# Kernel tuning notes

Measured on AMD Instinct MI355X. Metric: run time of the kernel, lower is better.

## Reference

```python
import jax, jax.numpy as jnp
import numpy as np

B, M, TP2, H, K, S = 64, 1, 1024, 256, 128, 1024
EPS = 2.220446049250313e-16  # numpy.finfo(float).eps


def setup_inputs() -> dict:
    key = jax.random.key(0)
    ks = jax.random.split(key, 12)
    inp = {
        'event': jax.random.randint(ks[0], (B, M, TP2), 0, K + 3),
        'dtime': jax.random.uniform(ks[1], (B, M, TP2), jnp.float32),
        'post': jax.random.uniform(ks[2], (B, M), jnp.float32),
        'duration': jax.random.uniform(ks[3], (B, M), jnp.float32),
        'dtime_sampling': jax.random.uniform(ks[4], (B, M, S), jnp.float32),
        'index_of_hidden_sampling': jax.random.randint(ks[5], (B, M, S), 0, B * M * (TP2 - 1)),
        'mask_sampling': jnp.ones((B, M, S), jnp.float32),
        # learned parameters
        'Emb': jax.random.normal(ks[6], (K + 3, H), jnp.float32) * 0.05,
        'W': jax.random.normal(ks[7], (7 * H, 2 * H), jnp.float32) * (1.0 / np.sqrt(2 * H)),
        'b': jnp.zeros((7 * H,), jnp.float32),
        'Wl': jax.random.normal(ks[8], (K, H), jnp.float32) * (1.0 / np.sqrt(H)),
    }
    return inp


def reference(event, dtime, post, duration, dtime_sampling, index_of_hidden_sampling,
              mask_sampling, Emb, W, b, Wl):
    Bs, Ms, Tp2 = event.shape
    Hd = Emb.shape[1]
    Tp1 = Tp2 - 1
    emb = Emb[event[:, :, :-1]]            # (B,M,T+1,H)
    dts = dtime[:, :, 1:]                  # (B,M,T+1)
    xs = (jnp.moveaxis(emb, 2, 0), jnp.moveaxis(dts, 2, 0))

    def step(carry, x):
        h, c, cbar = carry
        e, dt = x
        z = jnp.concatenate([e, h], axis=-1) @ W.T + b  # (B,M,7H)
        gi, gf, go, gz, gib, gfb, gd = jnp.split(z, 7, axis=-1)
        gi, gf, go = jax.nn.sigmoid(gi), jax.nn.sigmoid(gf), jax.nn.sigmoid(go)
        gib, gfb = jax.nn.sigmoid(gib), jax.nn.sigmoid(gfb)
        zc = jnp.tanh(gz)
        gd = jax.nn.softplus(gd)  # beta = 1
        c_i = gf * c + gi * zc
        cbar_i = gfb * cbar + gib * zc
        h_plus = go * jnp.tanh(c_i)  # decay with dtime = 0
        c_next = cbar_i + (c_i - cbar_i) * jnp.exp(-gd * dt[..., None])
        h_next = go * jnp.tanh(c_next)
        return (h_next, c_next, cbar_i), (c_i, cbar_i, gd, go, h_next)

    init = tuple(jnp.zeros((Bs, Ms, Hd), dtime.dtype) for _ in range(3))
    _, outs = jax.lax.scan(step, init, xs)
    all_c, all_cb, all_gd, all_go, all_h = (jnp.moveaxis(a, 0, 2) for a in outs)  # (B,M,T+1,H)

    # target + mask (getTarget)
    Kn = Wl.shape[0]
    tgt_raw = event[:, :, 1:]
    mask_complete = (tgt_raw < Kn).astype(dtime.dtype)
    tgt = jnp.where(tgt_raw < Kn, tgt_raw, 0)

    # log-intensity at events (getLogLambda)
    lam = jax.nn.softplus(all_h @ Wl.T)                        # (B,M,T+1,K)
    log_lam = jnp.log(lam + EPS)
    log_lam_tgt = jnp.take_along_axis(log_lam, tgt[..., None], axis=3)[..., 0] * mask_complete

    # sampled states (getSampledStates)
    idx = index_of_hidden_sampling.reshape(-1)
    Sn = dtime_sampling.shape[2]
    gather = lambda a: a.reshape(Bs * Ms * Tp1, Hd)[idx].reshape(Bs, Ms, Sn, Hd)
    cs, cbs, gds, gos = gather(all_c), gather(all_cb), gather(all_gd), gather(all_go)
    c_samp = cbs + (cs - cbs) * jnp.exp(-gds * dtime_sampling[..., None])
    hy = gos * jnp.tanh(c_samp)

    # MC integral (getIntegral)
    lam_s = jax.nn.softplus(hy @ Wl.T).sum(3)                  # (B,M,S)
    lam_mean = (lam_s * mask_sampling).sum(2) / mask_sampling.sum(2)
    integral = lam_mean * duration

    # complete log-likelihood per (batch, particle)
    loglik = log_lam_tgt.sum(2) - integral                     # (B,M)
    return loglik
```

## Files before the change

kernel.cpp:

```cpp
#include <hip/hip_runtime.h>
#include <hip/hip_fp16.h>
#include <cstdint>
#include <cstddef>

#define EPSF 2.220446049250313e-16f

#define Bn   64
#define TP2n 1024
#define Tn   1023
#define Hn   256
#define H7n  1792
#define Kn   128
#define NEn  131

typedef _Float16 f16x2 __attribute__((ext_vector_type(2)));
typedef unsigned uintx4 __attribute__((ext_vector_type(4)));

__device__ __forceinline__ f16x2 u2h(unsigned u) { return __builtin_bit_cast(f16x2, u); }
__device__ __forceinline__ f16x2 f2h(float f)    { return __builtin_bit_cast(f16x2, f); }

__device__ __forceinline__ int sdot4f(unsigned a, unsigned b, int c) {
#if __has_builtin(__builtin_amdgcn_sdot4)
  return __builtin_amdgcn_sdot4((int)a, (int)b, c, false);
#else
  int r = c;
#pragma unroll
  for (int i = 0; i < 4; ++i) {
    int av = ((int)(a << (24 - 8 * i))) >> 24;
    int bv = ((int)(b << (24 - 8 * i))) >> 24;
    r += av * bv;
  }
  return r;
#endif
}

__device__ __forceinline__ float sigmf(float x) { return 1.f / (1.f + __expf(-x)); }

__device__ __forceinline__ float tanhfast(float x) {
  float t = __expf(2.f * fabsf(x));
  float r = 1.f - 2.f / (t + 1.f);
  return copysignf(r, x);
}

__device__ __forceinline__ float softplusf(float x) {
  return fmaxf(x, 0.f) + log1pf(__expf(-fabsf(x)));
}

__device__ __host__ __forceinline__ int orig_row(int rp) {
  int role = rp / 448, i = rp % 448;
  return (i >> 6) * 256 + 64 * role + (i & 63);
}

__global__ __launch_bounds__(256) void k_ew(
    const float* __restrict__ Emb, const float* __restrict__ W,
    const float* __restrict__ bvec, float* __restrict__ EW) {
  const int e = blockIdx.x;
  const int chunk = blockIdx.y;
  const int tid = threadIdx.x;
  __shared__ float es[Hn];
  es[tid] = Emb[e * Hn + tid];
  __syncthreads();
  const int wv = tid >> 6, l = tid & 63;
  float4 ev = reinterpret_cast<const float4*>(es)[l];
  for (int i = 0; i < 28; ++i) {
    int rp = chunk * 112 + wv * 28 + i;
    int r = orig_row(rp);
    float4 wf = *reinterpret_cast<const float4*>(W + (size_t)r * 512 + 4 * l);
    float s = wf.x * ev.x + wf.y * ev.y + wf.z * ev.z + wf.w * ev.w;
#pragma unroll
    for (int off = 32; off; off >>= 1) s += __shfl_down(s, off);
    if (l == 0) EW[e * H7n + rp] = bvec[r] + s;
  }
}

__global__ __launch_bounds__(64) void k_wq4(const float* __restrict__ W,
                                            unsigned* __restrict__ wq,
                                            float* __restrict__ sc) {
  const int rp = blockIdx.x;
  const int r  = orig_row(rp);
  const int j  = threadIdx.x;
  const float* wr = W + (size_t)r * 512 + 256;
  float4 wv = *reinterpret_cast<const float4*>(wr + 4 * j);
  float m = fmaxf(fmaxf(fabsf(wv.x), fabsf(wv.y)),
                  fmaxf(fabsf(wv.z), fabsf(wv.w)));
#pragma unroll
  for (int off = 32; off; off >>= 1) m = fmaxf(m, __shfl_xor(m, off));
  float inv = (m > 0.f) ? 7.f / m : 0.f;
  if (j < 32) {
    float4 a = *reinterpret_cast<const float4*>(wr + 8 * j);
    float4 bq = *reinterpret_cast<const float4*>(wr + 8 * j + 4);
    float av[4] = {a.x, a.y, a.z, a.w};
    float bv[4] = {bq.x, bq.y, bq.z, bq.w};
    unsigned d = 0;
#pragma unroll
    for (int i = 0; i < 4; ++i) {
      unsigned qa = (unsigned)((int)rintf(fminf(fmaxf(av[i] * inv, -7.f), 7.f))) & 0xFu;
      unsigned qb = (unsigned)((int)rintf(fminf(fmaxf(bv[i] * inv, -7.f), 7.f))) & 0xFu;
      d |= (qa | (qb << 4)) << (8 * i);
    }
    wq[(size_t)rp * 32 + j] = d;
  }
  if (j == 0) sc[rp] = (m / 7.f) / (16.f * 127.f);
}

__global__ __launch_bounds__(64) void k_wlq(const float* __restrict__ Wl,
                                            unsigned* __restrict__ wlq,
                                            float* __restrict__ scl) {
  const int r = blockIdx.x;
  const int j = threadIdx.x;
  const float* row = Wl + (size_t)r * Hn;
  float4 v = reinterpret_cast<const float4*>(row)[j];
  float m = fmaxf(fmaxf(fabsf(v.x), fabsf(v.y)),
                  fmaxf(fabsf(v.z), fabsf(v.w)));
#pragma unroll
  for (int off = 32; off; off >>= 1) m = fmaxf(m, __shfl_xor(m, off));
  float inv = (m > 0.f) ? 127.f / m : 0.f;
  float vv[4] = {v.x, v.y, v.z, v.w};
  unsigned d = 0;
#pragma unroll
  for (int qi = 0; qi < 4; ++qi) {
    unsigned byte = (unsigned)((int)rintf(
        fminf(fmaxf(vv[qi] * inv, -127.f), 127.f))) & 255u;
    d |= byte << (8 * qi);
  }
  wlq[(((size_t)(j >> 2)) * 128 + r) * 4 + (j & 3)] = d;
  if (j == 0) scl[r] = m / (127.f * 127.f);
}

__global__ void k_init(float* __restrict__ acc, unsigned* __restrict__ hx) {
  int i = threadIdx.x;
  if (i < 192) acc[i] = 0.f;
  for (int k = i; k < Bn * 128; k += 1024) hx[k] = 1u;
}

__global__ __launch_bounds__(448) void k_scan(
    const int* __restrict__ event, const float* __restrict__ dtime,
    const float* __restrict__ EW, const unsigned* __restrict__ wq,
    const float* __restrict__ sc, unsigned* __restrict__ hx,
    uint2* __restrict__ state) {
  const int x = blockIdx.x;
  const int xcd = x & 7, q = x >> 3;
  const int b = xcd * 8 + (q >> 2);
  const int role = q & 3;
  const int tid = threadIdx.x;
  const int row = role * 448 + tid;

  __shared__ uintx4   wldsq[448 * 8];
  __shared__ float    zbuf[448];
  __shared__ uintx4   hds8q[16];
  __shared__ int      ev_s[TP2n];
  __shared__ float    dt_s[TP2n];
  unsigned* hds8 = reinterpret_cast<unsigned*>(hds8q);

  const float sc_r = sc[row];
  unsigned* hxb = hx + (size_t)b * 128;

  {
    const uintx4* src = reinterpret_cast<const uintx4*>(wq) +
                        (size_t)role * 448 * 8;
    for (int i = tid; i < 448 * 8; i += 448) {
      int r = i >> 3, g = i & 7;
      wldsq[g * 448 + r] = src[i];
    }
  }
  for (int i = tid; i < TP2n; i += 448) {
    ev_s[i] = event[b * TP2n + i];
    dt_s[i] = dtime[b * TP2n + i];
  }
  if (tid < 64) hds8[tid] = 0u;
  __syncthreads();

  float c_r = 0.f, cb_r = 0.f;
  const int j_u = 64 * role + tid;
  float ew_pf = EW[(size_t)ev_s[0] * H7n + row];

  for (int t = 0; t < Tn; ++t) {
    float ewc = ew_pf;
    ew_pf = EW[(size_t)ev_s[t + 1] * H7n + row];

    int acc0 = 0, acc1 = 0, acc2 = 0, acc3 = 0;
#pragma unroll
    for (int g = 0; g < 8; ++g) {
      uintx4 ww = wldsq[g * 448 + tid];
      uintx4 ha = hds8q[2 * g];
      uintx4 hb = hds8q[2 * g + 1];
      acc0 = sdot4f((ww[0] << 4) & 0xF0F0F0F0u, ha[0], acc0);
      acc1 = sdot4f( ww[0]       & 0xF0F0F0F0u, ha[1], acc1);
      acc2 = sdot4f((ww[1] << 4) & 0xF0F0F0F0u, ha[2], acc2);
      acc3 = sdot4f( ww[1]       & 0xF0F0F0F0u, ha[3], acc3);
      acc0 = sdot4f((ww[2] << 4) & 0xF0F0F0F0u, hb[0], acc0);
      acc1 = sdot4f( ww[2]       & 0xF0F0F0F0u, hb[1], acc1);
      acc2 = sdot4f((ww[3] << 4) & 0xF0F0F0F0u, hb[2], acc2);
      acc3 = sdot4f( ww[3]       & 0xF0F0F0F0u, hb[3], acc3);
    }
    zbuf[tid] = ewc + sc_r * (float)((acc0 + acc1) + (acc2 + acc3));
    __syncthreads();

    const unsigned parQ = (unsigned)(t & 1);
    const unsigned tauQ = (unsigned)((t >> 1) & 1);

    if (tid < 64) {
      float gi  = sigmf(zbuf[tid]);
      float gf  = sigmf(zbuf[64 + tid]);
      float go  = sigmf(zbuf[128 + tid]);
      float zc  = tanhfast(zbuf[192 + tid]);
      float gib = sigmf(zbuf[256 + tid]);
      float gfb = sigmf(zbuf[320 + tid]);
      float gd  = softplusf(zbuf[384 + tid]);
      float dt  = dt_s[t + 1];
      float ci  = gf * c_r + gi * zc;
      float cbi = gfb * cb_r + gib * zc;
      float cn  = cbi + (ci - cbi) * __expf(-gd * dt);
      float hn  = go * tanhfast(cn);
      c_r = cn; cb_r = cbi;
      unsigned bq = (unsigned)((int)rintf(
                        fminf(fmaxf(hn * 127.f, -127.f), 127.f))) & 255u;
      unsigned u0 = __shfl(bq, 4 * (tid & 15));
      unsigned u1 = __shfl(bq, 4 * (tid & 15) + 1);
      unsigned u2 = __shfl(bq, 4 * (tid & 15) + 2);
      unsigned u3 = __shfl(bq, 4 * (tid & 15) + 3);
      if (tid < 16) {
        unsigned d = u0 | (u1 << 8) | (u2 << 16) | (u3 << 24);
        hds8[16 * role + tid] = d;
        if (t < Tn - 1)
          __hip_atomic_store(hxb + parQ * 64 + 16 * role + tid,
                             (d & 0xFFFFFFFEu) | tauQ,
                             __ATOMIC_RELAXED, __HIP_MEMORY_SCOPE_AGENT);
      }
      f16x2 p0; p0[0] = (_Float16)ci; p0[1] = (_Float16)cbi;
      f16x2 p1; p1[0] = (_Float16)gd; p1[1] = (_Float16)go;
      uint2 o;
      o.x = __builtin_bit_cast(unsigned, p0);
      o.y = __builtin_bit_cast(unsigned, p1);
      state[((size_t)b * Tn + t) * Hn + j_u] = o;
    } else if (tid < 112 && t < Tn - 1) {
      int k  = tid - 64;
      int rr = (role + 1 + (k >> 4)) & 3;
      int m  = 16 * rr + (k & 15);
      unsigned v;
      do {
        v = __hip_atomic_load(hxb + parQ * 64 + m, __ATOMIC_RELAXED,
                              __HIP_MEMORY_SCOPE_AGENT);
      } while ((v & 1u) != tauQ);
      hds8[m] = v;
    }
    __syncthreads();
  }
}

__global__ __launch_bounds__(256) void k_post(
    const uint2* __restrict__ state, const int* __restrict__ event,
    const float* __restrict__ dtime, const float* __restrict__ Wl,
    float* __restrict__ loglik_sum) {
  const int b = blockIdx.y;
  const int wave = threadIdx.x >> 6;
  const int lane = threadIdx.x & 63;
  __shared__ float part[4];
  float acc = 0.f;
  for (int i = 0; i < 16; ++i) {
    const int t = blockIdx.x * 64 + wave * 16 + i;
    if (t >= Tn) break;
    const int tgt = event[b * TP2n + t + 1];
    if (tgt >= Kn) continue;
    const float dtv = dtime[b * TP2n + t + 1];
    const uint2* srow = state + ((size_t)b * Tn + t) * Hn;
    uint4 sA = *reinterpret_cast<const uint4*>(srow + lane * 4);
    uint4 sB = *reinterpret_cast<const uint4*>(srow + lane * 4 + 2);
    float4 wl = *reinterpret_cast<const float4*>(Wl + tgt * Hn + lane * 4);
    float h[4];
#pragma unroll
    for (int qq = 0; qq < 4; ++qq) {
      unsigned lo = (qq == 0) ? sA.x : (qq == 1) ? sA.z : (qq == 2) ? sB.x : sB.z;
      unsigned hi = (qq == 0) ? sA.y : (qq == 1) ? sA.w : (qq == 2) ? sB.y : sB.w;
      f16x2 p0 = u2h(lo), p1 = u2h(hi);
      float c = p0[0], cb = p0[1], gd = p1[0], go = p1[1];
      float cs = cb + (c - cb) * __expf(-gd * dtv);
      h[qq] = go * tanhfast(cs);
    }
    float d = h[0] * wl.x + h[1] * wl.y + h[2] * wl.z + h[3] * wl.w;
#pragma unroll
    for (int off = 32; off; off >>= 1) d += __shfl_down(d, off);
    if (lane == 0) acc += __logf(softplusf(d) + EPSF);
  }
  if (lane == 0) part[wave] = acc;
  __syncthreads();
  if (threadIdx.x == 0)
    atomicAdd(&loglik_sum[b], part[0] + part[1] + part[2] + part[3]);
}

__global__ __launch_bounds__(128) void k_samp(
    const uint2* __restrict__ state, const unsigned* __restrict__ wlq,
    const float* __restrict__ scl,
    const int* __restrict__ sidx, const float* __restrict__ sdt,
    const float* __restrict__ smask,
    float* __restrict__ lam_acc, float* __restrict__ mask_acc) {
  const int blk = blockIdx.x;
  const int b = blk >> 4;
  const int base = (b << 10) + (blk & 15) * 64;
  const int tid = threadIdx.x;

  __shared__ uintx4 wlt4[2048];
  __shared__ uintx4 hq4[16];
  __shared__ float  red[2];

  const uintx4* wg = reinterpret_cast<const uintx4*>(wlq);
  for (int i = tid; i < 2048; i += 128) wlt4[i] = wg[i];
  const float sc_row = scl[tid];
  float accl = 0.f, accm = 0.f;

  int   row = sidx[base];
  float dtv = sdt[base];
  float mk  = smask[base];
  uint4 st = *reinterpret_cast<const uint4*>(state + (size_t)row * Hn + 2 * tid);
  __syncthreads();

  for (int s = 0; s < 64; ++s) {
    f16x2 p0 = u2h(st.x), p1 = u2h(st.y);
    f16x2 q0 = u2h(st.z), q1 = u2h(st.w);
    float cs0 = (float)p0[1] + ((float)p0[0] - (float)p0[1]) * __expf(-(float)p1[0] * dtv);
    float cs1 = (float)q0[1] + ((float)q0[0] - (float)q0[1]) * __expf(-(float)q1[0] * dtv);
    float h0 = (float)p1[1] * tanhfast(cs0);
    float h1 = (float)q1[1] * tanhfast(cs1);
    unsigned i0 = (unsigned)((int)rintf(fminf(fmaxf(h0 * 127.f, -127.f), 127.f))) & 255u;
    unsigned i1 = (unsigned)((int)rintf(fminf(fmaxf(h1 * 127.f, -127.f), 127.f))) & 255u;
    unsigned p = i0 | (i1 << 8);
    unsigned pn = __shfl(p, tid + 1);
    if (!(tid & 1))
      reinterpret_cast<unsigned*>(hq4)[tid >> 1] = p | (pn << 16);

    uint4 st_n = st; float dt_n = dtv, mk_n = mk;
    if (s < 63) {
      int sg = base + s + 1;
      int r2 = sidx[sg];
      dt_n = sdt[sg];
      mk_n = smask[sg];
      st_n = *reinterpret_cast<const uint4*>(state + (size_t)r2 * Hn + 2 * tid);
    }
    __syncthreads();

    int acc = 0;
#pragma unroll
    for (int kg = 0; kg < 16; ++kg) {
      uintx4 w4 = wlt4[kg * 128 + tid];
      uintx4 h4 = hq4[kg];
      acc = sdot4f(w4[0], h4[0], acc);
      acc = sdot4f(w4[1], h4[1], acc);
      acc = sdot4f(w4[2], h4[2], acc);
      acc = sdot4f(w4[3], h4[3], acc);
    }
    float lam = softplusf(sc_row * (float)acc);
#pragma unroll
    for (int off = 32; off; off >>= 1) lam += __shfl_down(lam, off);
    if ((tid & 63) == 0) red[tid >> 6] = lam;
    __syncthreads();
    if (tid == 0) {
      accl += (red[0] + red[1]) * mk;
      accm += mk;
    }
    st = st_n; dtv = dt_n; mk = mk_n;
  }
  if (tid == 0) {
    atomicAdd(&lam_acc[b], accl);
    atomicAdd(&mask_acc[b], accm);
  }
}

__global__ void k_final(const float* __restrict__ loglik_sum,
                        const float* __restrict__ lam_acc,
                        const float* __restrict__ mask_acc,
                        const float* __restrict__ duration,
                        float* __restrict__ out) {
  int b = threadIdx.x;
  if (b < Bn) out[b] = loglik_sum[b] - (lam_acc[b] / mask_acc[b]) * duration[b];
}

extern "C" void kernel_launch(void* const* d_in, const int* in_sizes, int n_in,
                              void* d_out, int out_size, void* d_ws, size_t ws_size,
                              hipStream_t stream) {
  const int*   event    = (const int*)d_in[0];
  const float* dtime    = (const float*)d_in[1];
  const float* duration = (const float*)d_in[3];
  const float* sdt      = (const float*)d_in[4];
  const int*   sidx     = (const int*)d_in[5];
  const float* smask    = (const float*)d_in[6];
  const float* Emb      = (const float*)d_in[7];
  const float* W        = (const float*)d_in[8];
  const float* bv       = (const float*)d_in[9];
  const float* Wl       = (const float*)d_in[10];

  char* ws = (char*)d_ws;
  float*    EW         = (float*)(ws + 0);
  unsigned* wq         = (unsigned*)(ws + (1u << 20));
  float*    lam_acc    = (float*)(ws + (2u << 20));
  float*    mask_acc   = lam_acc + 64;
  float*    loglik_sum = lam_acc + 128;
  unsigned* hx         = (unsigned*)(ws + (2u << 20) + 8192);
  float*    sc         = (float*)(ws + (2u << 20) + 49152);
  unsigned* wlq        = (unsigned*)(ws + (2u << 20) + 131072);
  float*    scl        = (float*)(ws + (2u << 20) + 196608);
  uint2*    state      = (uint2*)(ws + (4u << 20));

  k_ew<<<dim3(NEn, 16), dim3(256), 0, stream>>>(Emb, W, bv, EW);
  k_wq4<<<dim3(H7n), dim3(64), 0, stream>>>(W, wq, sc);
  k_wlq<<<dim3(Kn), dim3(64), 0, stream>>>(Wl, wlq, scl);
  k_init<<<dim3(1), dim3(1024), 0, stream>>>(lam_acc, hx);
  k_scan<<<dim3(256), dim3(448), 0, stream>>>(event, dtime, EW, wq, sc, hx,
                                              state);
  k_post<<<dim3(16, 64), dim3(256), 0, stream>>>(state, event, dtime, Wl,
                                                 loglik_sum);
  k_samp<<<dim3(1024), dim3(128), 0, stream>>>(state, wlq, scl, sidx, sdt,
                                               smask, lam_acc, mask_acc);
  k_final<<<dim3(1), dim3(64), 0, stream>>>(loglik_sum, lam_acc, mask_acc,
                                            duration, (float*)d_out);
}
```

Baseline: 2.308 ms.

## Switch recurrent weights to int8 and read them from global memory in scan

The recurrent weight quantization moves from packed int4 to int8 with a matching scale, so the scan's inner dot product drops the nibble unpacking shifts and masks. The weights, now twice as large, are no longer staged in LDS; each thread reads its row from global memory every timestep through the cache. This cuts ALU work per step and LDS use, at the risk of global or L2 latency landing on the serial critical path.

```diff
diff --git a/kernel.cpp b/kernel.cpp
--- a/kernel.cpp
+++ b/kernel.cpp
@@ -73,7 +73,7 @@
   }
 }
 
-__global__ __launch_bounds__(64) void k_wq4(const float* __restrict__ W,
+__global__ __launch_bounds__(64) void k_wq8(const float* __restrict__ W,
                                             unsigned* __restrict__ wq,
                                             float* __restrict__ sc) {
   const int rp = blockIdx.x;
@@ -85,22 +85,17 @@
                   fmaxf(fabsf(wv.z), fabsf(wv.w)));
 #pragma unroll
   for (int off = 32; off; off >>= 1) m = fmaxf(m, __shfl_xor(m, off));
-  float inv = (m > 0.f) ? 7.f / m : 0.f;
-  if (j < 32) {
-    float4 a = *reinterpret_cast<const float4*>(wr + 8 * j);
-    float4 bq = *reinterpret_cast<const float4*>(wr + 8 * j + 4);
-    float av[4] = {a.x, a.y, a.z, a.w};
-    float bv[4] = {bq.x, bq.y, bq.z, bq.w};
-    unsigned d = 0;
-#pragma unroll
-    for (int i = 0; i < 4; ++i) {
-      unsigned qa = (unsigned)((int)rintf(fminf(fmaxf(av[i] * inv, -7.f), 7.f))) & 0xFu;
-      unsigned qb = (unsigned)((int)rintf(fminf(fmaxf(bv[i] * inv, -7.f), 7.f))) & 0xFu;
-      d |= (qa | (qb << 4)) << (8 * i);
-    }
-    wq[(size_t)rp * 32 + j] = d;
-  }
-  if (j == 0) sc[rp] = (m / 7.f) / (16.f * 127.f);
+  float inv = (m > 0.f) ? 127.f / m : 0.f;
+  float v[4] = {wv.x, wv.y, wv.z, wv.w};
+  unsigned d = 0;
+#pragma unroll
+  for (int q = 0; q < 4; ++q) {
+    float s = fminf(fmaxf(v[q] * inv, -127.f), 127.f);
+    unsigned byte = (unsigned)((int)rintf(s)) & 255u;
+    d |= byte << (8 * q);
+  }
+  wq[(size_t)rp * 64 + j] = d;
+  if (j == 0) sc[rp] = m / (127.f * 127.f);
 }
 
 __global__ __launch_bounds__(64) void k_wlq(const float* __restrict__ Wl,
@@ -145,24 +140,16 @@
   const int tid = threadIdx.x;
   const int row = role * 448 + tid;
 
-  __shared__ uintx4   wldsq[448 * 8];
   __shared__ float    zbuf[448];
   __shared__ uintx4   hds8q[16];
   __shared__ int      ev_s[TP2n];
   __shared__ float    dt_s[TP2n];
   unsigned* hds8 = reinterpret_cast<unsigned*>(hds8q);
 
-  const float sc_r = sc[row];
+  const uintx4* wp = reinterpret_cast<const uintx4*>(wq) + (size_t)row * 16;
+  const float  sc_r = sc[row];
   unsigned* hxb = hx + (size_t)b * 128;
 
-  {
-    const uintx4* src = reinterpret_cast<const uintx4*>(wq) +
-                        (size_t)role * 448 * 8;
-    for (int i = tid; i < 448 * 8; i += 448) {
-      int r = i >> 3, g = i & 7;
-      wldsq[g * 448 + r] = src[i];
-    }
-  }
   for (int i = tid; i < TP2n; i += 448) {
     ev_s[i] = event[b * TP2n + i];
     dt_s[i] = dtime[b * TP2n + i];
@@ -180,18 +167,13 @@
 
     int acc0 = 0, acc1 = 0, acc2 = 0, acc3 = 0;
 #pragma unroll
-    for (int g = 0; g < 8; ++g) {
-      uintx4 ww = wldsq[g * 448 + tid];
-      uintx4 ha = hds8q[2 * g];
-      uintx4 hb = hds8q[2 * g + 1];
-      acc0 = sdot4f((ww[0] << 4) & 0xF0F0F0F0u, ha[0], acc0);
-      acc1 = sdot4f( ww[0]       & 0xF0F0F0F0u, ha[1], acc1);
-      acc2 = sdot4f((ww[1] << 4) & 0xF0F0F0F0u, ha[2], acc2);
-      acc3 = sdot4f( ww[1]       & 0xF0F0F0F0u, ha[3], acc3);
-      acc0 = sdot4f((ww[2] << 4) & 0xF0F0F0F0u, hb[0], acc0);
-      acc1 = sdot4f( ww[2]       & 0xF0F0F0F0u, hb[1], acc1);
-      acc2 = sdot4f((ww[3] << 4) & 0xF0F0F0F0u, hb[2], acc2);
-      acc3 = sdot4f( ww[3]       & 0xF0F0F0F0u, hb[3], acc3);
+    for (int i = 0; i < 16; ++i) {
+      uintx4 ww = wp[i];
+      uintx4 hh = hds8q[i];
+      acc0 = sdot4f(ww[0], hh[0], acc0);
+      acc1 = sdot4f(ww[1], hh[1], acc1);
+      acc2 = sdot4f(ww[2], hh[2], acc2);
+      acc3 = sdot4f(ww[3], hh[3], acc3);
     }
     zbuf[tid] = ewc + sc_r * (float)((acc0 + acc1) + (acc2 + acc3));
     __syncthreads();
@@ -401,7 +383,7 @@
   uint2*    state      = (uint2*)(ws + (4u << 20));
 
   k_ew<<<dim3(NEn, 16), dim3(256), 0, stream>>>(Emb, W, bv, EW);
-  k_wq4<<<dim3(H7n), dim3(64), 0, stream>>>(W, wq, sc);
+  k_wq8<<<dim3(H7n), dim3(64), 0, stream>>>(W, wq, sc);
   k_wlq<<<dim3(Kn), dim3(64), 0, stream>>>(Wl, wlq, scl);
   k_init<<<dim3(1), dim3(1024), 0, stream>>>(lam_acc, hx);
   k_scan<<<dim3(256), dim3(448), 0, stream>>>(event, dtime, EW, wq, sc, hx,
```

After: 1.997 ms, median of 2. 1.16x faster.
